# Performance work log

Hardware: AMD Instinct MI355X
Metric: run time of the kernel (lower is better)

The kernel has to match this reference:

```python
import jax, jax.numpy as jnp
import numpy as np

NEG_SLOPE = 0.2


def gat_layer(x, src, dst, W, a_src, a_dst, b, concat):
    # x: [N, F_in], W: [F_in, H*C], a_src/a_dst: [H, C], b: [H*C] or [C]
    N = x.shape[0]
    H, C = a_src.shape
    h = (x @ W).reshape(N, H, C)                       # per-head projections
    al_s = jnp.einsum('nhc,hc->nh', h, a_src)          # [N, H]
    al_d = jnp.einsum('nhc,hc->nh', h, a_dst)          # [N, H]
    e = jax.nn.leaky_relu(al_s[src] + al_d[dst], NEG_SLOPE)  # [E, H]
    # softmax over incoming edges of each destination node
    m = jax.ops.segment_max(e, dst, num_segments=N)    # [N, H]
    ex = jnp.exp(e - m[dst])
    s = jax.ops.segment_sum(ex, dst, num_segments=N)   # [N, H]
    alpha = ex / (s[dst] + 1e-16)                      # [E, H]
    msg = h[src] * alpha[:, :, None]                   # [E, H, C]
    out = jax.ops.segment_sum(msg, dst, num_segments=N)  # [N, H, C]
    out = out.reshape(N, H * C) if concat else out.mean(axis=1)
    return out + b


def setup_inputs() -> dict:
    key = jax.random.key(0)
    ks = jax.random.split(key, 12)
    N, E, F_in, HID, H, NCLS = 100000, 1600000, 128, 32, 4, 40
    x = jax.random.normal(ks[0], (N, F_in), dtype=jnp.float32)
    edge_index = jax.random.randint(ks[1], (2, E), 0, N, dtype=jnp.int32)
    W1 = jax.random.normal(ks[2], (F_in, H * HID), dtype=jnp.float32) * 0.1
    as1 = jax.random.normal(ks[3], (H, HID), dtype=jnp.float32) * 0.1
    ad1 = jax.random.normal(ks[4], (H, HID), dtype=jnp.float32) * 0.1
    b1 = jnp.zeros((H * HID,), dtype=jnp.float32)
    W2 = jax.random.normal(ks[5], (H * HID, H * NCLS), dtype=jnp.float32) * 0.1
    as2 = jax.random.normal(ks[6], (H, NCLS), dtype=jnp.float32) * 0.1
    ad2 = jax.random.normal(ks[7], (H, NCLS), dtype=jnp.float32) * 0.1
    b2 = jnp.zeros((NCLS,), dtype=jnp.float32)
    return {"x": x, "edge_index": edge_index, "W1": W1, "as1": as1,
            "ad1": ad1, "b1": b1, "W2": W2, "as2": as2, "ad2": ad2, "b2": b2}


def reference(x, edge_index, W1, as1, ad1, b1, W2, as2, ad2, b2):
    src, dst = edge_index[0], edge_index[1]
    h = gat_layer(x, src, dst, W1, as1, ad1, b1, concat=True)
    h = jax.nn.relu(h)  # dropout=0.0 -> identity
    out = gat_layer(h, src, dst, W2, as2, ad2, b2, concat=False)
    return jax.nn.log_softmax(out, axis=-1)
```

## Files before the change

### kernel.cpp

```cpp
#include <hip/hip_runtime.h>

typedef short short8 __attribute__((ext_vector_type(8)));
typedef float f32x4 __attribute__((ext_vector_type(4)));
typedef int   i32x4 __attribute__((ext_vector_type(4)));
typedef unsigned short u16;
typedef unsigned int u32;

__device__ __forceinline__ float b2f(u16 u){ union{u32 i; float f;} v; v.i=((u32)u)<<16; return v.f; }
__device__ __forceinline__ u16 f2b(float f){ union{float f; u32 i;} v; v.f=f; return (u16)((v.i + 0x7fffu + ((v.i>>16)&1u))>>16); }
__device__ __forceinline__ float loadv(const void* p, long i, bool isbf){
  return isbf ? b2f(((const u16*)p)[i]) : ((const float*)p)[i];
}

__global__ void detect_bf16(const void* x, int n, int* flag){
  __shared__ int cnt;
  if (threadIdx.x==0) cnt = 0;
  __syncthreads();
  int m = n < 4096 ? n : 4096;
  int good = 0;
  for (int i = threadIdx.x; i < m; i += 256){
    u16 u = ((const u16*)x)[i];
    int e = (u >> 7) & 0xff;
    if (u == 0 || (e >= 100 && e <= 140)) good++;
  }
  atomicAdd(&cnt, good);
  __syncthreads();
  if (threadIdx.x==0){
    flag[0] = (cnt >= (m*3)/4) ? 1 : 0;
    flag[1] = 1;
  }
}

__global__ __launch_bounds__(256) void convw(const void* __restrict__ W, u16* __restrict__ WT,
                                             int M, const int* __restrict__ flag){
  const bool wbf = *flag != 0;
  int i = blockIdx.x*256 + threadIdx.x;
  if (i >= 128*M) return;
  int k = i / M, c = i - k*M;
  WT[c*128 + k] = wbf ? ((const u16*)W)[i] : f2b(((const float*)W)[i]);
}

__global__ __launch_bounds__(256) void count_x(const int* __restrict__ dst,
    int* __restrict__ counts, int E, int N, int nchunk){
  int r = blockIdx.x & 7;
  int chunk = blockIdx.x >> 3;
  int lo = (int)(((long)N * r) >> 3);
  int hi = (int)(((long)N * (r+1)) >> 3);
  int per = (E + nchunk - 1) / nchunk;
  int s = chunk * per, t = min(E, s + per);
  for (int e = s + threadIdx.x; e < t; e += 256){
    int d = dst[e];
    if (d >= lo && d < hi) atomicAdd(&counts[d], 1);
  }
}

__global__ __launch_bounds__(256) void scatter_x(const int* __restrict__ src, const int* __restrict__ dst,
    const int* __restrict__ rp, int* __restrict__ cur,
    int* __restrict__ psrc, int E, int N, int nchunk){
  int r = blockIdx.x & 7;
  int chunk = blockIdx.x >> 3;
  int lo = (int)(((long)N * r) >> 3);
  int hi = (int)(((long)N * (r+1)) >> 3);
  int per = (E + nchunk - 1) / nchunk;
  int s = chunk * per, t = min(E, s + per);
  for (int e = s + threadIdx.x; e < t; e += 256){
    int d = dst[e];
    if (d >= lo && d < hi){
      int pos = rp[d] + atomicAdd(&cur[d], 1);
      psrc[pos] = src[e];
    }
  }
}

__global__ __launch_bounds__(256) void scan_bsum(const int* __restrict__ counts, int* __restrict__ bsum, int N){
  __shared__ int sm[256];
  int t = threadIdx.x, i = blockIdx.x*256 + t;
  sm[t] = (i < N) ? counts[i] : 0;
  __syncthreads();
  for (int off = 128; off; off >>= 1){
    if (t < off) sm[t] += sm[t+off];
    __syncthreads();
  }
  if (t == 0) bsum[blockIdx.x] = sm[0];
}

__global__ __launch_bounds__(1024) void scan_top(const int* __restrict__ bsum, int* __restrict__ bscan, int B){
  __shared__ int sm[1024];
  int t = threadIdx.x;
  int v = (t < B) ? bsum[t] : 0;
  sm[t] = v;
  __syncthreads();
  for (int off = 1; off < 1024; off <<= 1){
    int x = (t >= off) ? sm[t-off] : 0;
    __syncthreads();
    sm[t] += x;
    __syncthreads();
  }
  if (t < B) bscan[t] = sm[t] - v;
}

__global__ __launch_bounds__(256) void scan_final(const int* __restrict__ counts, const int* __restrict__ bscan,
                                                  int* __restrict__ rp, int N, int E){
  __shared__ int sm[256];
  int t = threadIdx.x, i = blockIdx.x*256 + t;
  int v = (i < N) ? counts[i] : 0;
  sm[t] = v;
  __syncthreads();
  for (int off = 1; off < 256; off <<= 1){
    int x = (t >= off) ? sm[t-off] : 0;
    __syncthreads();
    sm[t] += x;
    __syncthreads();
  }
  if (i < N) rp[i] = bscan[blockIdx.x] + sm[t] - v;
  if (i == 0) rp[N] = E;
}

template<int M>
__global__ __launch_bounds__(256) void gemm_k(const void* __restrict__ X, const u16* __restrict__ WT,
                                              u16* __restrict__ OUT, u16* __restrict__ OUT2, int N,
                                              const int* __restrict__ flagX){
  __shared__ u16 wt[M][136];
  const bool xbf = *flagX != 0;
  int tid = threadIdx.x;
  for (int i = tid; i < M*16; i += 256){
    int c = i >> 4, k8 = (i & 15) << 3;
    *(short8*)&wt[c][k8] = *(const short8*)&WT[c*128 + k8];
  }
  __syncthreads();
  int wave = tid >> 6, lane = tid & 63;
  int quad = lane >> 4, l16 = lane & 15;
  int rowbase = blockIdx.x*64 + wave*16;
  int rr = rowbase + l16; if (rr >= N) rr = N-1;
  const int NT = M/16;
  f32x4 acc[NT];
  #pragma unroll
  for (int t=0;t<NT;t++) acc[t] = (f32x4){0.f,0.f,0.f,0.f};
  #pragma unroll
  for (int kt = 0; kt < 4; kt++){
    int kb = kt*32 + quad*8;
    short8 a;
    if (xbf){
      a = *(const short8*)((const u16*)X + (size_t)rr*128 + kb);
    } else {
      const float* xf = (const float*)X + (size_t)rr*128 + kb;
      #pragma unroll
      for (int j=0;j<8;j++) a[j] = (short)f2b(xf[j]);
    }
    #pragma unroll
    for (int t=0;t<NT;t++){
      short8 b = *(const short8*)&wt[t*16 + l16][kb];
      acc[t] = __builtin_amdgcn_mfma_f32_16x16x32_bf16(a, b, acc[t], 0, 0, 0);
    }
  }
  #pragma unroll
  for (int t=0;t<NT;t++){
    #pragma unroll
    for (int r=0;r<4;r++){
      int row = rowbase + quad*4 + r;
      if (row < N){
        u16 val = f2b(acc[t][r]);
        if (M > 128 && t*16 >= 128) OUT2[(size_t)row*32 + (t*16 - 128) + l16] = val;
        else                        OUT [(size_t)row*128 + t*16 + l16]        = val;
      }
    }
  }
}

template<int C>
__global__ __launch_bounds__(256) void al_k(const u16* __restrict__ Hm, const void* __restrict__ as_,
                     const void* __restrict__ ad_,
                     float* __restrict__ als, float* __restrict__ ald, int N, const int* __restrict__ flag){
  __shared__ float s_as[4*C], s_ad[4*C];
  const bool isbf = *flag != 0;
  for (int i = threadIdx.x; i < 4*C; i += 256){
    s_as[i] = loadv(as_, i, isbf);
    s_ad[i] = loadv(ad_, i, isbf);
  }
  __syncthreads();
  int idx = blockIdx.x*256 + threadIdx.x;
  if (idx >= N*4) return;
  int n = idx >> 2, h = idx & 3;
  const short8* row = (const short8*)(Hm + (size_t)n*(4*C) + h*C);
  float ss = 0.f, sd = 0.f;
  #pragma unroll
  for (int v = 0; v < C/8; v++){
    short8 pk = row[v];
    #pragma unroll
    for (int j = 0; j < 8; j++){
      union{u32 i; float f;} u; u.i = ((u32)(u16)pk[j]) << 16;
      ss += u.f * s_as[h*C + v*8 + j];
      sd += u.f * s_ad[h*C + v*8 + j];
    }
  }
  als[idx] = ss;
  ald[idx] = sd;
}

__global__ __launch_bounds__(256) void al2_k(const u16* __restrict__ Hm, const u16* __restrict__ Ht,
                     const void* __restrict__ as_, const void* __restrict__ ad_,
                     float* __restrict__ als, float* __restrict__ ald, int N, const int* __restrict__ flag){
  __shared__ float s_as[160], s_ad[160];
  const bool isbf = *flag != 0;
  for (int i = threadIdx.x; i < 160; i += 256){
    s_as[i] = loadv(as_, i, isbf);
    s_ad[i] = loadv(ad_, i, isbf);
  }
  __syncthreads();
  int idx = blockIdx.x*256 + threadIdx.x;
  if (idx >= N*4) return;
  int n = idx >> 2, h = idx & 3;
  float ss = 0.f, sd = 0.f;
  int c0 = h*40;
  #pragma unroll
  for (int v = 0; v < 5; v++){
    int c = c0 + v*8;
    const u16* p = (c < 128) ? (Hm + (size_t)n*128 + c) : (Ht + (size_t)n*32 + (c - 128));
    short8 pk = *(const short8*)p;
    #pragma unroll
    for (int j = 0; j < 8; j++){
      union{u32 i; float f;} u; u.i = ((u32)(u16)pk[j]) << 16;
      ss += u.f * s_as[c + j];
      sd += u.f * s_ad[c + j];
    }
  }
  als[idx] = ss;
  ald[idx] = sd;
}

__global__ __launch_bounds__(256) void agg1(const u16* __restrict__ h1,
    const float* __restrict__ als, const float* __restrict__ ald, const void* __restrict__ b1,
    const int* __restrict__ rp, const int* __restrict__ psrc,
    u16* __restrict__ hrelu, int N, const int* __restrict__ flag){
  __shared__ __align__(16) int   sbuf[4][16];
  __shared__ __align__(16) float ebT[4][4*20];
  const bool isbf = *flag != 0;
  int wave = threadIdx.x >> 6, lane = threadIdx.x & 63;
  int node = blockIdx.x*4 + wave;
  bool live = node < N;
  int nd = live ? node : 0;
  int hd = lane >> 4;
  int eidx = lane >> 2, hA = lane & 3;
  int beg = __builtin_amdgcn_readfirstlane(rp[nd]);
  int end = __builtin_amdgcn_readfirstlane(rp[nd+1]);
  if (!live){ beg = 0; end = 0; }
  float advA = ald[nd*4 + hA];
  const char* hb = (const char*)h1;
  int lane4 = lane << 2;
  int* sb = sbuf[wave];
  float* eb = ebT[wave];
  float a0 = 0.f, a1 = 0.f;
  float sp = 0.f;
  for (int cbeg = beg; cbeg < end; cbeg += 16){
    int cnt = min(16, end - cbeg);
    int e = cbeg + eidx;
    bool vv = e < end;
    int ec = vv ? e : beg;
    int s = psrc[ec];
    float lv = als[s*4 + hA] + advA;
    lv = fmaxf(lv, 0.2f*lv);
    float ex = vv ? __expf(lv) : 0.f;
    sp += ex;
    eb[hA*20 + eidx] = ex;
    if (hA == 0) sb[eidx] = vv ? (s << 8) : 0;
    for (int j0 = 0; j0 < cnt; j0 += 4){
      i32x4 off4 = *(const i32x4*)&sb[j0];
      f32x4 ex4  = *(const f32x4*)&eb[hd*20 + j0];
      u32 p[4];
      #pragma unroll
      for (int i=0;i<4;i++) p[i] = *(const u32*)(hb + (u32)(off4[i] + lane4));
      #pragma unroll
      for (int i=0;i<4;i++){
        union{u32 u; float f;} w;
        w.u = p[i] << 16;         a0 += ex4[i]*w.f;
        w.u = p[i] & 0xffff0000u; a1 += ex4[i]*w.f;
      }
    }
  }
  sp += __shfl_xor(sp, 4);  sp += __shfl_xor(sp, 8);
  sp += __shfl_xor(sp, 16); sp += __shfl_xor(sp, 32);
  float sum = __shfl(sp, hd);
  if (live){
    float inv = 1.f/(sum + 1e-16f);
    float v0 = a0*inv + loadv(b1, 2*lane,     isbf);
    float v1 = a1*inv + loadv(b1, 2*lane + 1, isbf);
    v0 = v0 > 0.f ? v0 : 0.f;
    v1 = v1 > 0.f ? v1 : 0.f;
    u32 packed = (u32)f2b(v0) | ((u32)f2b(v1) << 16);
    *(u32*)(hrelu + (size_t)node*128 + 2*lane) = packed;
  }
}

__global__ __launch_bounds__(256) void agg2(const u16* __restrict__ h2m, const u16* __restrict__ h2t,
    const float* __restrict__ als, const float* __restrict__ ald, const void* __restrict__ b2,
    const int* __restrict__ rp, const int* __restrict__ psrc,
    void* __restrict__ out, int N, const int* __restrict__ flag){
  __shared__ __align__(16) int   sbuf[4][16];
  __shared__ __align__(16) float ebT[4][4*20];
  __shared__ __align__(16) float sm[4][160];
  const bool isbf = *flag != 0;
  int wave = threadIdx.x >> 6, lane = threadIdx.x & 63;
  int node = blockIdx.x*4 + wave;
  bool live = node < N;
  int nd = live ? node : 0;
  int g = lane >> 4, s = lane & 15;
  int hm = s / 5;
  int moff = s << 4;
  int tof  = s << 2;
  int eidx = lane >> 2, hA = lane & 3;
  int beg = __builtin_amdgcn_readfirstlane(rp[nd]);
  int end = __builtin_amdgcn_readfirstlane(rp[nd+1]);
  if (!live){ beg = 0; end = 0; }
  float advA = ald[nd*4 + hA];
  const char* hbm = (const char*)h2m;
  const char* hbt = (const char*)h2t;
  int* sb = sbuf[wave];
  float* eb = ebT[wave];
  float am[8] = {0.f,0.f,0.f,0.f,0.f,0.f,0.f,0.f};
  float at0 = 0.f, at1 = 0.f;
  float sp = 0.f;
  for (int cbeg = beg; cbeg < end; cbeg += 16){
    int cnt = min(16, end - cbeg);
    int e = cbeg + eidx;
    bool vv = e < end;
    int ec = vv ? e : beg;
    int src = psrc[ec];
    float lv = als[src*4 + hA] + advA;
    lv = fmaxf(lv, 0.2f*lv);
    float ex = vv ? __expf(lv) : 0.f;
    sp += ex;
    eb[hA*20 + eidx] = ex;
    if (hA == 0) sb[eidx] = vv ? src : 0;
    for (int j0 = 0; j0 < cnt; j0 += 4){
      int sv    = sb[j0 + g];
      float exm = eb[hm*20 + j0 + g];
      float ext = eb[3*20  + j0 + g];
      i32x4 P = *(const i32x4*)(hbm + ((((u32)sv) << 8) + moff));
      u32   q = *(const u32*) (hbt + ((((u32)sv) << 6) + tof));
      union{u32 u; float f;} w;
      #pragma unroll
      for (int i=0;i<4;i++){
        u32 pv = (u32)P[i];
        w.u = pv << 16;         am[2*i]   += exm*w.f;
        w.u = pv & 0xffff0000u; am[2*i+1] += exm*w.f;
      }
      w.u = q << 16;         at0 += ext*w.f;
      w.u = q & 0xffff0000u; at1 += ext*w.f;
    }
  }
  sp += __shfl_xor(sp, 4);  sp += __shfl_xor(sp, 8);
  sp += __shfl_xor(sp, 16); sp += __shfl_xor(sp, 32);
  float Sm = __shfl(sp, hm);
  float S3 = __shfl(sp, 3);
  #pragma unroll
  for (int k=0;k<8;k++){ am[k] += __shfl_xor(am[k],16); am[k] += __shfl_xor(am[k],32); }
  at0 += __shfl_xor(at0,16); at0 += __shfl_xor(at0,32);
  at1 += __shfl_xor(at1,16); at1 += __shfl_xor(at1,32);
  if (lane < 16){
    float invm = 1.f/(Sm + 1e-16f);
    float invt = 1.f/(S3 + 1e-16f);
    f32x4 v0 = {am[0]*invm, am[1]*invm, am[2]*invm, am[3]*invm};
    f32x4 v1 = {am[4]*invm, am[5]*invm, am[6]*invm, am[7]*invm};
    *(f32x4*)&sm[wave][8*s]     = v0;
    *(f32x4*)&sm[wave][8*s + 4] = v1;
    sm[wave][128 + 2*s] = at0*invt;
    sm[wave][129 + 2*s] = at1*invt;
  }
  __syncthreads();
  float v = -__builtin_inff();
  if (lane < 40)
    v = (sm[wave][lane] + sm[wave][40+lane] + sm[wave][80+lane] + sm[wave][120+lane]) * 0.25f
        + loadv(b2, lane, isbf);
  float mxo = v;
  for (int o = 32; o; o >>= 1) mxo = fmaxf(mxo, __shfl_xor(mxo, o));
  float exl = (lane < 40) ? __expf(v - mxo) : 0.f;
  float S = exl;
  for (int o = 32; o; o >>= 1) S += __shfl_xor(S, o);
  if (live && lane < 40){
    float r = v - mxo - __logf(S);
    if (isbf) ((u16*)out)[(size_t)node*40 + lane] = f2b(r);
    else      ((float*)out)[(size_t)node*40 + lane] = r;
  }
}

extern "C" void kernel_launch(void* const* d_in, const int* in_sizes, int n_in,
                              void* d_out, int out_size, void* d_ws, size_t ws_size,
                              hipStream_t stream){
  const void* x   = d_in[0];
  const int*  ei  = (const int*)d_in[1];
  const void* W1  = d_in[2];
  const void* as1 = d_in[3];
  const void* ad1 = d_in[4];
  const void* b1  = d_in[5];
  const void* W2  = d_in[6];
  const void* as2 = d_in[7];
  const void* ad2 = d_in[8];
  const void* b2  = d_in[9];

  const int N = in_sizes[0] / 128;
  const int E = in_sizes[1] / 2;
  const int* esrc = ei;
  const int* edst = ei + E;

  char* w = (char*)d_ws;
  size_t off = 0;
  auto take = [&](size_t bytes)->void*{
    void* p = w + off;
    off = (off + bytes + 255) & ~(size_t)255;
    return p;
  };
  u16*   h12    = (u16*)take((size_t)N*128*2);
  u16*   h2t    = (u16*)take((size_t)N*32*2);
  u16*   hrelu  = (u16*)take((size_t)N*128*2);
  float* als1   = (float*)take((size_t)N*4*4);
  float* ald1   = (float*)take((size_t)N*4*4);
  float* als2   = (float*)take((size_t)N*4*4);
  float* ald2   = (float*)take((size_t)N*4*4);
  int*   rowptr = (int*)take((size_t)(N+1)*4);
  int*   counts = (int*)take((size_t)N*4);
  int*   bsum   = (int*)take(1024*4);
  int*   bscan  = (int*)take(1024*4);
  int*   psrc   = (int*)take((size_t)E*4);
  int*   flag   = (int*)take(64);
  u16*   wt1    = (u16*)take(128*128*2);
  u16*   wt2    = (u16*)take(160*128*2);

  const int B = (N + 255) / 256;
  const int NCHUNK = 128;

  detect_bf16<<<1, 256, 0, stream>>>(x, N*128, flag);
  convw<<<(128*128+255)/256, 256, 0, stream>>>(W1, wt1, 128, flag);
  convw<<<(128*160+255)/256, 256, 0, stream>>>(W2, wt2, 160, flag);

  hipMemsetAsync(counts, 0, (size_t)N*4, stream);
  count_x<<<8*NCHUNK, 256, 0, stream>>>(edst, counts, E, N, NCHUNK);
  scan_bsum<<<B, 256, 0, stream>>>(counts, bsum, N);
  scan_top<<<1, 1024, 0, stream>>>(bsum, bscan, B);
  scan_final<<<B, 256, 0, stream>>>(counts, bscan, rowptr, N, E);
  hipMemsetAsync(counts, 0, (size_t)N*4, stream);
  scatter_x<<<8*NCHUNK, 256, 0, stream>>>(esrc, edst, rowptr, counts, psrc, E, N, NCHUNK);

  gemm_k<128><<<(N+63)/64, 256, 0, stream>>>(x, wt1, h12, h2t , N, flag);
  al_k<32><<<(4*N+255)/256, 256, 0, stream>>>(h12, as1, ad1, als1, ald1, N, flag);
  agg1<<<(N+3)/4, 256, 0, stream>>>(h12, als1, ald1, b1, rowptr, psrc, hrelu, N, flag);

  gemm_k<160><<<(N+63)/64, 256, 0, stream>>>(hrelu, wt2, h12, h2t, N, flag+1);
  al2_k<<<(4*N+255)/256, 256, 0, stream>>>(h12, h2t, as2, ad2, als2, ald2, N, flag);
  agg2<<<(N+3)/4, 256, 0, stream>>>(h12, h2t, als2, ald2, b2, rowptr, psrc, d_out, N, flag);
}
```

Baseline: 486.5 us.

## Fuse attention logit computation into GEMM epilogue and merge init kernels

Computes the per-head source/destination attention dot products inside the GEMM epilogue from the fp32 MFMA accumulators, using cross-lane shuffle reductions. This removes the separate al_k/al2_k kernels and their re-read of the bf16 projection. It also merges the two weight-conversion kernels and the first counts memset into one init kernel, and clears counts inside scan_final instead of with a second memset. Fewer launches and less memory traffic, at the cost of more registers and shuffles in the GEMM. Logits now come from unrounded fp32 values, so results may differ slightly.

Result: no change. 480.4 us (-1.3%).

```diff
diff --git a/kernel.cpp b/kernel.cpp
--- a/kernel.cpp
+++ b/kernel.cpp
@@ -31,13 +31,21 @@
   }
 }
 
-__global__ __launch_bounds__(256) void convw(const void* __restrict__ W, u16* __restrict__ WT,
-                                             int M, const int* __restrict__ flag){
+__global__ __launch_bounds__(256) void init_k(const void* __restrict__ W1, const void* __restrict__ W2,
+                                              u16* __restrict__ WT1, u16* __restrict__ WT2,
+                                              int* __restrict__ counts, int N, const int* __restrict__ flag){
   const bool wbf = *flag != 0;
-  int i = blockIdx.x*256 + threadIdx.x;
-  if (i >= 128*M) return;
-  int k = i / M, c = i - k*M;
-  WT[c*128 + k] = wbf ? ((const u16*)W)[i] : f2b(((const float*)W)[i]);
+  int gid = blockIdx.x*256 + threadIdx.x;
+  if (gid < 128*128){
+    int i = gid, k = i >> 7, c = i & 127;
+    WT1[c*128 + k] = wbf ? ((const u16*)W1)[i] : f2b(((const float*)W1)[i]);
+  } else if (gid < 128*128 + 128*160){
+    int i = gid - 128*128, k = i / 160, c = i - k*160;
+    WT2[c*128 + k] = wbf ? ((const u16*)W2)[i] : f2b(((const float*)W2)[i]);
+  } else {
+    int i = gid - (128*128 + 128*160);
+    if (i < N) counts[i] = 0;
+  }
 }
 
 __global__ __launch_bounds__(256) void count_x(const int* __restrict__ dst,
@@ -99,11 +107,12 @@
   if (t < B) bscan[t] = sm[t] - v;
 }
 
-__global__ __launch_bounds__(256) void scan_final(const int* __restrict__ counts, const int* __restrict__ bscan,
+__global__ __launch_bounds__(256) void scan_final(const int* __restrict__ counts_in, int* __restrict__ counts_clr,
+                                                  const int* __restrict__ bscan,
                                                   int* __restrict__ rp, int N, int E){
   __shared__ int sm[256];
   int t = threadIdx.x, i = blockIdx.x*256 + t;
-  int v = (i < N) ? counts[i] : 0;
+  int v = (i < N) ? counts_in[i] : 0;
   sm[t] = v;
   __syncthreads();
   for (int off = 1; off < 256; off <<= 1){
@@ -112,20 +121,28 @@
     sm[t] += x;
     __syncthreads();
   }
-  if (i < N) rp[i] = bscan[blockIdx.x] + sm[t] - v;
+  if (i < N){ rp[i] = bscan[blockIdx.x] + sm[t] - v; counts_clr[i] = 0; }
   if (i == 0) rp[N] = E;
 }
 
-template<int M>
-__global__ __launch_bounds__(256) void gemm_k(const void* __restrict__ X, const u16* __restrict__ WT,
-                                              u16* __restrict__ OUT, u16* __restrict__ OUT2, int N,
-                                              const int* __restrict__ flagX){
+template<int M, int C>
+__global__ __launch_bounds__(256) void gemm_al(const void* __restrict__ X, const u16* __restrict__ WT,
+                                               const void* __restrict__ as_, const void* __restrict__ ad_,
+                                               u16* __restrict__ OUT, u16* __restrict__ OUT2,
+                                               float* __restrict__ als, float* __restrict__ ald,
+                                               int N, const int* __restrict__ flagX, const int* __restrict__ flagW){
   __shared__ u16 wt[M][136];
+  __shared__ float s_as[4*C], s_ad[4*C];
   const bool xbf = *flagX != 0;
+  const bool abf = *flagW != 0;
   int tid = threadIdx.x;
   for (int i = tid; i < M*16; i += 256){
     int c = i >> 4, k8 = (i & 15) << 3;
     *(short8*)&wt[c][k8] = *(const short8*)&WT[c*128 + k8];
+  }
+  for (int i = tid; i < 4*C; i += 256){
+    s_as[i] = loadv(as_, i, abf);
+    s_ad[i] = loadv(ad_, i, abf);
   }
   __syncthreads();
   int wave = tid >> 6, lane = tid & 63;
@@ -165,67 +182,51 @@
       }
     }
   }
-}
-
-template<int C>
-__global__ __launch_bounds__(256) void al_k(const u16* __restrict__ Hm, const void* __restrict__ as_,
-                     const void* __restrict__ ad_,
-                     float* __restrict__ als, float* __restrict__ ald, int N, const int* __restrict__ flag){
-  __shared__ float s_as[4*C], s_ad[4*C];
-  const bool isbf = *flag != 0;
-  for (int i = threadIdx.x; i < 4*C; i += 256){
-    s_as[i] = loadv(as_, i, isbf);
-    s_ad[i] = loadv(ad_, i, isbf);
-  }
-  __syncthreads();
-  int idx = blockIdx.x*256 + threadIdx.x;
-  if (idx >= N*4) return;
-  int n = idx >> 2, h = idx & 3;
-  const short8* row = (const short8*)(Hm + (size_t)n*(4*C) + h*C);
-  float ss = 0.f, sd = 0.f;
-  #pragma unroll
-  for (int v = 0; v < C/8; v++){
-    short8 pk = row[v];
+  float ps[4][4], pd[4][4];
+  #pragma unroll
+  for (int r=0;r<4;r++)
     #pragma unroll
-    for (int j = 0; j < 8; j++){
-      union{u32 i; float f;} u; u.i = ((u32)(u16)pk[j]) << 16;
-      ss += u.f * s_as[h*C + v*8 + j];
-      sd += u.f * s_ad[h*C + v*8 + j];
-    }
-  }
-  als[idx] = ss;
-  ald[idx] = sd;
-}
-
-__global__ __launch_bounds__(256) void al2_k(const u16* __restrict__ Hm, const u16* __restrict__ Ht,
-                     const void* __restrict__ as_, const void* __restrict__ ad_,
-                     float* __restrict__ als, float* __restrict__ ald, int N, const int* __restrict__ flag){
-  __shared__ float s_as[160], s_ad[160];
-  const bool isbf = *flag != 0;
-  for (int i = threadIdx.x; i < 160; i += 256){
-    s_as[i] = loadv(as_, i, isbf);
-    s_ad[i] = loadv(ad_, i, isbf);
-  }
-  __syncthreads();
-  int idx = blockIdx.x*256 + threadIdx.x;
-  if (idx >= N*4) return;
-  int n = idx >> 2, h = idx & 3;
-  float ss = 0.f, sd = 0.f;
-  int c0 = h*40;
-  #pragma unroll
-  for (int v = 0; v < 5; v++){
-    int c = c0 + v*8;
-    const u16* p = (c < 128) ? (Hm + (size_t)n*128 + c) : (Ht + (size_t)n*32 + (c - 128));
-    short8 pk = *(const short8*)p;
+    for (int h=0;h<4;h++){ ps[r][h]=0.f; pd[r][h]=0.f; }
+  #pragma unroll
+  for (int t=0;t<NT;t++){
+    const int hlo = (t*16)/C;
+    const int hhi = (t*16+15)/C;
+    int col = t*16 + l16;
+    float avs = s_as[col], avd = s_ad[col];
+    if (hlo == hhi){
+      #pragma unroll
+      for (int r=0;r<4;r++){ ps[r][hlo] += acc[t][r]*avs; pd[r][hlo] += acc[t][r]*avd; }
+    } else {
+      if (l16 < hhi*C - t*16){
+        #pragma unroll
+        for (int r=0;r<4;r++){ ps[r][hlo] += acc[t][r]*avs; pd[r][hlo] += acc[t][r]*avd; }
+      } else {
+        #pragma unroll
+        for (int r=0;r<4;r++){ ps[r][hhi] += acc[t][r]*avs; pd[r][hhi] += acc[t][r]*avd; }
+      }
+    }
+  }
+  #pragma unroll
+  for (int off=1; off<16; off<<=1){
     #pragma unroll
-    for (int j = 0; j < 8; j++){
-      union{u32 i; float f;} u; u.i = ((u32)(u16)pk[j]) << 16;
-      ss += u.f * s_as[c + j];
-      sd += u.f * s_ad[c + j];
-    }
-  }
-  als[idx] = ss;
-  ald[idx] = sd;
+    for (int r=0;r<4;r++)
+      #pragma unroll
+      for (int h=0;h<4;h++){
+        ps[r][h] += __shfl_xor(ps[r][h], off);
+        pd[r][h] += __shfl_xor(pd[r][h], off);
+      }
+  }
+  float vs = 0.f, vd = 0.f;
+  #pragma unroll
+  for (int r=0;r<4;r++)
+    #pragma unroll
+    for (int h=0;h<4;h++)
+      if (l16 == r*4 + h){ vs = ps[r][h]; vd = pd[r][h]; }
+  int wrow = rowbase + quad*4 + (l16 >> 2);
+  if (wrow < N){
+    als[wrow*4 + (l16 & 3)] = vs;
+    ald[wrow*4 + (l16 & 3)] = vd;
+  }
 }
 
 __global__ __launch_bounds__(256) void agg1(const u16* __restrict__ h1,
@@ -427,24 +428,22 @@
 
   const int B = (N + 255) / 256;
   const int NCHUNK = 128;
+  const int INIT_W = 128*128 + 128*160;
 
   detect_bf16<<<1, 256, 0, stream>>>(x, N*128, flag);
-  convw<<<(128*128+255)/256, 256, 0, stream>>>(W1, wt1, 128, flag);
-  convw<<<(128*160+255)/256, 256, 0, stream>>>(W2, wt2, 160, flag);
-
-  hipMemsetAsync(counts, 0, (size_t)N*4, stream);
+  init_k<<<(INIT_W + N + 255)/256, 256, 0, stream>>>(W1, W2, wt1, wt2, counts, N, flag);
+
   count_x<<<8*NCHUNK, 256, 0, stream>>>(edst, counts, E, N, NCHUNK);
   scan_bsum<<<B, 256, 0, stream>>>(counts, bsum, N);
   scan_top<<<1, 1024, 0, stream>>>(bsum, bscan, B);
-  scan_final<<<B, 256, 0, stream>>>(counts, bscan, rowptr, N, E);
-  hipMemsetAsync(counts, 0, (size_t)N*4, stream);
+  scan_final<<<B, 256, 0, stream>>>(counts, counts, bscan, rowptr, N, E);
   scatter_x<<<8*NCHUNK, 256, 0, stream>>>(esrc, edst, rowptr, counts, psrc, E, N, NCHUNK);
 
-  gemm_k<128><<<(N+63)/64, 256, 0, stream>>>(x, wt1, h12, h2t , N, flag);
-  al_k<32><<<(4*N+255)/256, 256, 0, stream>>>(h12, as1, ad1, als1, ald1, N, flag);
+  gemm_al<128,32><<<(N+63)/64, 256, 0, stream>>>(x, wt1, as1, ad1, h12, h2t ,
+                                                 als1, ald1, N, flag, flag);
   agg1<<<(N+3)/4, 256, 0, stream>>>(h12, als1, ald1, b1, rowptr, psrc, hrelu, N, flag);
 
-  gemm_k<160><<<(N+63)/64, 256, 0, stream>>>(hrelu, wt2, h12, h2t, N, flag+1);
-  al2_k<<<(4*N+255)/256, 256, 0, stream>>>(h12, h2t, as2, ad2, als2, ald2, N, flag);
+  gemm_al<160,40><<<(N+63)/64, 256, 0, stream>>>(hrelu, wt2, as2, ad2, h12, h2t,
+                                                 als2, ald2, N, flag+1, flag);
   agg2<<<(N+3)/4, 256, 0, stream>>>(h12, h2t, als2, ald2, b2, rowptr, psrc, d_out, N, flag);
 }
```
